# Optimization experiments

Hardware: AMD Instinct MI355X
Metric: run time of the kernel (lower is better)

The kernel has to match this reference:

```python
import jax, jax.numpy as jnp
import numpy as np

N_NODES = 32768
N_EDGES = 524288
EPS = 1e-5

def _layernorm(h):
    mu = jnp.mean(h, axis=-1, keepdims=True)
    var = jnp.var(h, axis=-1, keepdims=True)
    return (h - mu) / jnp.sqrt(var + EPS)

def _leaky_relu(h):
    return jnp.where(h >= 0, h, 0.01 * h)

def setup_inputs() -> dict:
    key = jax.random.key(0)
    ks = jax.random.split(key, 16)
    F, H, D = 256, 256, 1024
    x = jax.random.normal(ks[0], (N_NODES, F), dtype=jnp.float32)
    src = jax.random.randint(ks[1], (N_EDGES,), 0, N_NODES, dtype=jnp.int32)
    dst = jax.random.randint(ks[2], (N_EDGES,), 0, N_NODES, dtype=jnp.int32)
    dims = [F, H, H, H, D]
    params = {}
    for i in range(4):
        params[f"W{i+1}"] = jax.random.normal(ks[3 + i], (dims[i], dims[i + 1]), dtype=jnp.float32) * (1.0 / np.sqrt(dims[i]))
        params[f"b{i+1}"] = jnp.zeros((dims[i + 1],), dtype=jnp.float32)
    Wm = jax.random.normal(ks[8], (D, D), dtype=jnp.float32) * (1.0 / np.sqrt(D))
    bm = jnp.zeros((D,), dtype=jnp.float32)
    Ws = jax.random.normal(ks[9], (D, D), dtype=jnp.float32) * (1.0 / np.sqrt(D))
    bs = jnp.zeros((D,), dtype=jnp.float32)
    return dict(x=x, src=src, dst=dst, W1=params["W1"], b1=params["b1"], W2=params["W2"], b2=params["b2"], W3=params["W3"], b3=params["b3"], W4=params["W4"], b4=params["b4"], Wm=Wm, bm=bm, Ws=Ws, bs=bs, batch_b=128, nodes_per=256)

def reference(x, src, dst, W1, b1, W2, b2, W3, b3, W4, b4, Wm, bm, Ws, bs, batch_b, nodes_per):
    # DGL GraphConv norm='both': out = D_in^{-1/2} * A @ (D_out^{-1/2} * h) @ W + b
    ones = jnp.ones((src.shape[0],), dtype=x.dtype)
    out_deg = jax.ops.segment_sum(ones, src, num_segments=N_NODES)
    in_deg = jax.ops.segment_sum(ones, dst, num_segments=N_NODES)
    ns = jnp.where(out_deg > 0, jax.lax.rsqrt(out_deg), 1.0)[:, None]
    nd = jnp.where(in_deg > 0, jax.lax.rsqrt(in_deg), 1.0)[:, None]

    def gconv(h, W, b):
        if W.shape[0] <= W.shape[1]:  # aggregate first, then project (in <= out)
            m = (h * ns)[src]
            agg = jax.ops.segment_sum(m, dst, num_segments=N_NODES) * nd
            return agg @ W + b
        else:  # project first
            h = (h * ns) @ W
            agg = jax.ops.segment_sum(h[src], dst, num_segments=N_NODES) * nd
            return agg + b

    h = x
    for (W, b) in [(W1, b1), (W2, b2), (W3, b3), (W4, b4)]:
        h = _layernorm(_leaky_relu(gconv(h, W, b)))
    h = h.reshape(batch_b, nodes_per, -1)  # [B, N_per, D]
    h = jnp.mean(h, axis=1)                # AvePool over nodes
    h = _layernorm(h)
    mean = h @ Wm + bm
    log_std = h @ Ws + bs
    return (mean, log_std)
```

## Files before the change

kernel.cpp:

```cpp
#include <hip/hip_runtime.h>

#define N_NODES 32768
#define N_EDGES 524288

typedef __attribute__((ext_vector_type(8))) short short8;
typedef __attribute__((ext_vector_type(4))) float floatx4;

#define GLOBAL_AS __attribute__((address_space(1)))
#define LDS_AS __attribute__((address_space(3)))

__device__ __forceinline__ unsigned short f2bf(float x) {
    union { float f; unsigned u; } v; v.f = x;
    unsigned r = v.u + 0x7FFF + ((v.u >> 16) & 1);
    return (unsigned short)(r >> 16);
}
__device__ __forceinline__ float bf2f(unsigned short u) {
    union { unsigned u; float f; } v; v.u = ((unsigned)u) << 16;
    return v.f;
}


__global__ __launch_bounds__(256) void k_hist(const int* __restrict__ src,
                                              const int* __restrict__ dst,
                                              unsigned int* __restrict__ histOut32,
                                              unsigned int* __restrict__ histIn32) {
    __shared__ unsigned int hOut[8192];
    __shared__ unsigned int hIn[8192];
    int t = threadIdx.x, b = blockIdx.x;
    for (int i = t; i < 8192; i += 256) { hOut[i] = 0; hIn[i] = 0; }
    __syncthreads();
    int base = b * 4096;
    for (int i = t; i < 4096; i += 256) {
        int s = src[base + i], d = dst[base + i];
        atomicAdd(&hOut[s >> 2], 1u << ((s & 3) * 8));
        atomicAdd(&hIn[d >> 2], 1u << ((d & 3) * 8));
    }
    __syncthreads();
    for (int i = t; i < 8192; i += 256) {
        histOut32[b * 8192 + i] = hOut[i];
        histIn32[b * 8192 + i] = hIn[i];
    }
}

__global__ __launch_bounds__(256) void k_merge(const unsigned int* __restrict__ histOut32,
                                               const unsigned int* __restrict__ histIn32,
                                               unsigned int* __restrict__ pre32,
                                               int* __restrict__ in_deg,
                                               float* __restrict__ ns,
                                               float* __restrict__ nd) {
    int g = blockIdx.x * 256 + threadIdx.x;
    int ri0 = 0, ri1 = 0, ri2 = 0, ri3 = 0;
    for (int b = 0; b < 128; b++) {
        pre32[b * 8192 + g] = (unsigned)ri0 | ((unsigned)ri1 << 8) |
                              ((unsigned)ri2 << 16) | ((unsigned)ri3 << 24);
        unsigned int v = histIn32[b * 8192 + g];
        ri0 += v & 255; ri1 += (v >> 8) & 255; ri2 += (v >> 16) & 255; ri3 += (v >> 24) & 255;
    }
    in_deg[g * 4 + 0] = ri0; in_deg[g * 4 + 1] = ri1;
    in_deg[g * 4 + 2] = ri2; in_deg[g * 4 + 3] = ri3;
    nd[g * 4 + 0] = ri0 > 0 ? rsqrtf((float)ri0) : 1.0f;
    nd[g * 4 + 1] = ri1 > 0 ? rsqrtf((float)ri1) : 1.0f;
    nd[g * 4 + 2] = ri2 > 0 ? rsqrtf((float)ri2) : 1.0f;
    nd[g * 4 + 3] = ri3 > 0 ? rsqrtf((float)ri3) : 1.0f;
    int ro0 = 0, ro1 = 0, ro2 = 0, ro3 = 0;
    for (int b = 0; b < 128; b++) {
        unsigned int v = histOut32[b * 8192 + g];
        ro0 += v & 255; ro1 += (v >> 8) & 255; ro2 += (v >> 16) & 255; ro3 += (v >> 24) & 255;
    }
    ns[g * 4 + 0] = ro0 > 0 ? rsqrtf((float)ro0) : 1.0f;
    ns[g * 4 + 1] = ro1 > 0 ? rsqrtf((float)ro1) : 1.0f;
    ns[g * 4 + 2] = ro2 > 0 ? rsqrtf((float)ro2) : 1.0f;
    ns[g * 4 + 3] = ro3 > 0 ? rsqrtf((float)ro3) : 1.0f;
}

__global__ void k_scan(const int* __restrict__ in_deg, int* __restrict__ row_ptr) {
    __shared__ int part[1024];
    int t = threadIdx.x;
    int base = t * 32;
    int local[32];
    int s = 0;
    for (int i = 0; i < 32; i++) { local[i] = s; s += in_deg[base + i]; }
    part[t] = s;
    __syncthreads();
    for (int off = 1; off < 1024; off <<= 1) {
        int v = (t >= off) ? part[t - off] : 0;
        __syncthreads();
        part[t] += v;
        __syncthreads();
    }
    int prev = (t == 0) ? 0 : part[t - 1];
    for (int i = 0; i < 32; i++) row_ptr[base + i] = prev + local[i];
    if (t == 1023) row_ptr[N_NODES] = part[1023];
}

__global__ __launch_bounds__(256) void k_place(const int* __restrict__ src,
                                               const int* __restrict__ dst,
                                               const unsigned int* __restrict__ pre32,
                                               const int* __restrict__ row_ptr,
                                               int* __restrict__ csr_src) {
    __shared__ unsigned int cur[8192];
    int t = threadIdx.x, b = blockIdx.x;
    for (int i = t; i < 8192; i += 256) cur[i] = 0;
    __syncthreads();
    int base = b * 4096;
    const unsigned int* preb = pre32 + b * 8192;
    for (int i = t; i < 4096; i += 256) {
        int s = src[base + i], d = dst[base + i];
        int sh = (d & 3) * 8;
        unsigned int old = atomicAdd(&cur[d >> 2], 1u << sh);
        int rank = (old >> sh) & 255;
        int pb = (preb[d >> 2] >> sh) & 255;
        csr_src[row_ptr[d] + pb + rank] = s;
    }
}

struct TransDescs {
    const float* W[6];
    unsigned short* Wt[6];
    int K[6], N[6];
    int end[6];
};

__global__ __launch_bounds__(256) void k_transpose_all(TransDescs d) {
    int id = blockIdx.x, s = 0;
#pragma unroll
    for (int i = 0; i < 6; i++) if (id >= d.end[i]) s = i + 1;
    int base = (s == 0) ? 0 : d.end[s - 1];
    int t = id - base;
    int K = d.K[s], N = d.N[s];
    int ncols = N >> 5;
    int n0 = (t % ncols) * 32, k0 = (t / ncols) * 32;
    const float* W = d.W[s];
    unsigned short* Wt = d.Wt[s];
    __shared__ float tile[32][33];
    int tx = threadIdx.x & 31, ty = threadIdx.x >> 5;
    for (int r = 0; r < 32; r += 8)
        tile[ty + r][tx] = W[(size_t)(k0 + ty + r) * N + n0 + tx];
    __syncthreads();
    for (int r = 0; r < 32; r += 8)
        Wt[(size_t)(n0 + ty + r) * K + k0 + tx] = f2bf(tile[tx][ty + r]);
}

__global__ __launch_bounds__(256) void k_scale_x(const float* __restrict__ x,
                                                 const float* __restrict__ ns,
                                                 unsigned short* __restrict__ xsb) {
    int i = blockIdx.x * 256 + threadIdx.x;
    float4 v = ((const float4*)x)[i];
    int n = i >> 6;
    int f = (i & 63) * 4;
    float sc = ns[n];
    ushort4 o;
    o.x = f2bf(v.x * sc); o.y = f2bf(v.y * sc);
    o.z = f2bf(v.z * sc); o.w = f2bf(v.w * sc);
    size_t off = (size_t)(f >> 6) * (N_NODES * 64) + (size_t)n * 64 + (f & 63);
    *(ushort4*)(xsb + off) = o;
}

__global__ __launch_bounds__(128, 8) void k_aggregate(
        const unsigned short* __restrict__ hs,
        const int* __restrict__ row_ptr,
        const int* __restrict__ csr_src,
        const float* __restrict__ nd,
        unsigned short* __restrict__ aggb) {
    __shared__ int eIdx[512];
    __shared__ int rp[17];
    const int tid = threadIdx.x;
    const int n0 = blockIdx.x * 16;
    if (tid <= 16) rp[tid] = row_ptr[n0 + tid];
    __syncthreads();
    const int ebeg = rp[0];
    const int ecount = rp[16] - ebeg;
    const int ecached = ecount < 512 ? ecount : 512;
    for (int i = tid; i < ecached; i += 128) eIdx[i] = csr_src[ebeg + i];
    __syncthreads();

    const int nl = tid >> 3;
    const int fs = tid & 7;
    const int n = n0 + nl;
    const int beg = rp[nl] - ebeg, end = rp[nl + 1] - ebeg;
    const float sc = nd[n];

    auto sweep = [&](auto fetch) {
        for (int c = 0; c < 4; c++) {
            const unsigned short* hp = hs + (size_t)c * (N_NODES * 64) + fs * 8;
            float acc[8];
#pragma unroll
            for (int k = 0; k < 8; k++) acc[k] = 0.f;
            int e = beg;
            for (; e + 8 <= end; e += 8) {
                int s0 = fetch(e),     s1 = fetch(e + 1), s2 = fetch(e + 2), s3 = fetch(e + 3);
                int s4 = fetch(e + 4), s5 = fetch(e + 5), s6 = fetch(e + 6), s7 = fetch(e + 7);
                short8 v0 = *(const short8*)(hp + (size_t)s0 * 64);
                short8 v1 = *(const short8*)(hp + (size_t)s1 * 64);
                short8 v2 = *(const short8*)(hp + (size_t)s2 * 64);
                short8 v3 = *(const short8*)(hp + (size_t)s3 * 64);
                short8 v4 = *(const short8*)(hp + (size_t)s4 * 64);
                short8 v5 = *(const short8*)(hp + (size_t)s5 * 64);
                short8 v6 = *(const short8*)(hp + (size_t)s6 * 64);
                short8 v7 = *(const short8*)(hp + (size_t)s7 * 64);
#pragma unroll
                for (int k = 0; k < 8; k++)
                    acc[k] += ((bf2f((unsigned short)v0[k]) + bf2f((unsigned short)v1[k])) +
                               (bf2f((unsigned short)v2[k]) + bf2f((unsigned short)v3[k]))) +
                              ((bf2f((unsigned short)v4[k]) + bf2f((unsigned short)v5[k])) +
                               (bf2f((unsigned short)v6[k]) + bf2f((unsigned short)v7[k])));
            }
            for (; e + 2 <= end; e += 2) {
                int s0 = fetch(e), s1 = fetch(e + 1);
                short8 v0 = *(const short8*)(hp + (size_t)s0 * 64);
                short8 v1 = *(const short8*)(hp + (size_t)s1 * 64);
#pragma unroll
                for (int k = 0; k < 8; k++)
                    acc[k] += bf2f((unsigned short)v0[k]) + bf2f((unsigned short)v1[k]);
            }
            if (e < end) {
                int s = fetch(e);
                short8 v = *(const short8*)(hp + (size_t)s * 64);
#pragma unroll
                for (int k = 0; k < 8; k++) acc[k] += bf2f((unsigned short)v[k]);
            }
            short8 o;
#pragma unroll
            for (int k = 0; k < 8; k++) o[k] = (short)f2bf(acc[k] * sc);
            __builtin_nontemporal_store(o, (short8*)(aggb + (size_t)n * 256 + c * 64 + fs * 8));
        }
    };
    if (ecount <= 512)
        sweep([&](int e) { return eIdx[e]; });
    else
        sweep([&](int e) { return csr_src[ebeg + e]; });
}

__global__ __launch_bounds__(256, 2) void gemm_ln(
        const unsigned short* __restrict__ A, const unsigned short* __restrict__ Bt,
        const float* __restrict__ bias, const float* __restrict__ ns,
        unsigned short* __restrict__ hsb) {
    __shared__ __align__(16) unsigned short As[2][64 * 32];
    __shared__ __align__(16) unsigned short Bs[2][256 * 32];
    __shared__ float sSum[2][64], sSum2[2][64], sMa[64], sMb[64];
    const int tid = threadIdx.x;
    const int lane = tid & 63;
    const int w = tid >> 6;
    const int wr = (w >> 1) * 32;
    const int wc = (w & 1) * 128;
    const int rowBase = blockIdx.x * 64;
    const int K = 256;

    floatx4 acc[2][8];
#pragma unroll
    for (int i = 0; i < 2; i++)
#pragma unroll
        for (int j = 0; j < 8; j++) acc[i][j] = (floatx4){0.f, 0.f, 0.f, 0.f};

    const int pr = lane >> 3;
    const int uu = (lane & 7) ^ pr;
    const int rowInGrp = pr * 2 + (uu >> 2);
    const int kc = (uu & 3) * 8;
    const unsigned short* gA = A + (size_t)(rowBase + w * 16 + rowInGrp) * K + kc;
    const unsigned short* gB = Bt + (size_t)(w * 64 + rowInGrp) * K + kc;
    const int aBase = (w * 16) * 32;
    const int bBase = (w * 64) * 32;

    const int q = lane >> 4;
    const int ln = lane & 15;
    const int uf = (((ln & 1) << 2) | q) ^ ((ln >> 1) & 7);

#define STAGE(buf_, koff_)                                                               \
    {                                                                                    \
        unsigned short* lA = As[buf_] + aBase;                                           \
        unsigned short* lB = Bs[buf_] + bBase;                                           \
        __builtin_amdgcn_global_load_lds((const GLOBAL_AS short*)(gA + (koff_)),         \
                                         (LDS_AS short*)lA, 16, 0, 0);                   \
        __builtin_amdgcn_global_load_lds((const GLOBAL_AS short*)(gB + (koff_)),         \
                                         (LDS_AS short*)lB, 16, 0, 0);                   \
        __builtin_amdgcn_global_load_lds((const GLOBAL_AS short*)(gB + (koff_) + (size_t)16 * K), \
                                         (LDS_AS short*)(lB + 16 * 32), 16, 0, 0);       \
        __builtin_amdgcn_global_load_lds((const GLOBAL_AS short*)(gB + (koff_) + (size_t)32 * K), \
                                         (LDS_AS short*)(lB + 32 * 32), 16, 0, 0);       \
        __builtin_amdgcn_global_load_lds((const GLOBAL_AS short*)(gB + (koff_) + (size_t)48 * K), \
                                         (LDS_AS short*)(lB + 48 * 32), 16, 0, 0);       \
    }

    STAGE(0, 0)
    int buf = 0;
    for (int k0 = 0; k0 < K; k0 += 32) {
        __syncthreads();
        if (k0 + 32 < K) STAGE(buf ^ 1, k0 + 32)
        const unsigned short* rA = As[buf];
        const unsigned short* rB = Bs[buf];
        short8 af[2], bfr[8];
#pragma unroll
        for (int i = 0; i < 2; i++)
            af[i] = *(const short8*)(rA + (((wr + i * 16 + ln) >> 1) << 6) + uf * 8);
#pragma unroll
        for (int j = 0; j < 8; j++)
            bfr[j] = *(const short8*)(rB + (((wc + j * 16 + ln) >> 1) << 6) + uf * 8);
#pragma unroll
        for (int i = 0; i < 2; i++)
#pragma unroll
            for (int j = 0; j < 8; j++)
                acc[i][j] = __builtin_amdgcn_mfma_f32_16x16x32_bf16(af[i], bfr[j], acc[i][j], 0, 0, 0);
        buf ^= 1;
    }
#undef STAGE

    float bcol[8];
#pragma unroll
    for (int j = 0; j < 8; j++) bcol[j] = bias[wc + j * 16 + ln];
    const int wcIdx = w & 1;
#pragma unroll
    for (int i = 0; i < 2; i++) {
#pragma unroll
        for (int r = 0; r < 4; r++) {
            float s = 0.f, s2 = 0.f;
#pragma unroll
            for (int j = 0; j < 8; j++) {
                float v = acc[i][j][r] + bcol[j];
                v = v >= 0.f ? v : 0.01f * v;
                s += v; s2 += v * v;
            }
#pragma unroll
            for (int off = 8; off > 0; off >>= 1) {
                s += __shfl_down(s, off, 16);
                s2 += __shfl_down(s2, off, 16);
            }
            if (ln == 0) {
                int row = wr + i * 16 + q * 4 + r;
                sSum[wcIdx][row] = s;
                sSum2[wcIdx][row] = s2;
            }
        }
    }
    __syncthreads();
    if (tid < 64) {
        float mu = (sSum[0][tid] + sSum[1][tid]) * (1.0f / 256.0f);
        float var = (sSum2[0][tid] + sSum2[1][tid]) * (1.0f / 256.0f) - mu * mu;
        float rs = rsqrtf(var + 1e-5f);
        float nsv = ns[rowBase + tid];
        sMa[tid] = rs * nsv;
        sMb[tid] = -mu * rs * nsv;
    }
    __syncthreads();
#pragma unroll
    for (int i = 0; i < 2; i++) {
#pragma unroll
        for (int r = 0; r < 4; r++) {
            int row = wr + i * 16 + q * 4 + r;
            float a = sMa[row], bb = sMb[row];
#pragma unroll
            for (int j = 0; j < 8; j++) {
                float v = acc[i][j][r] + bcol[j];
                v = v >= 0.f ? v : 0.01f * v;
                int col = wc + j * 16 + ln;
                size_t off = (size_t)(col >> 6) * (N_NODES * 64) +
                             (size_t)(rowBase + row) * 64 + (col & 63);
                hsb[off] = f2bf(v * a + bb);
            }
        }
    }
}

template <bool LEAKY, bool OUT_BF16>
__global__ __launch_bounds__(256) void gemm_mfma(
        const unsigned short* __restrict__ A, const unsigned short* __restrict__ Bt,
        const float* __restrict__ bias,
        void* __restrict__ Cv,
        int M, int N, int K) {
    __shared__ __align__(16) unsigned short As[2][128 * 32];
    __shared__ __align__(16) unsigned short Bs[2][128 * 32];
    const int tid = threadIdx.x;
    const int lane = tid & 63;
    const int w = tid >> 6;
    const int wr = (w >> 1) * 64;
    const int wc = (w & 1) * 64;
    const int rowBase = blockIdx.x * 128;
    const int colBase = blockIdx.y * 128;

    floatx4 acc[4][4];
#pragma unroll
    for (int i = 0; i < 4; i++)
#pragma unroll
        for (int j = 0; j < 4; j++) acc[i][j] = (floatx4){0.f, 0.f, 0.f, 0.f};

    const int pr = lane >> 3;
    const int uu = (lane & 7) ^ pr;
    const int srow = w * 32 + pr * 2 + (uu >> 2);
    const int kc = (uu & 3) * 8;
    const unsigned short* gA = A + (size_t)(rowBase + srow) * K + kc;
    const unsigned short* gB = Bt + (size_t)(colBase + srow) * K + kc;
    const int wbase = (w * 32) * 32;

    const int q = lane >> 4;
    const int ln = lane & 15;
    const int uf = (((ln & 1) << 2) | q) ^ ((ln >> 1) & 7);

    {
        unsigned short* lA = As[0] + wbase;
        unsigned short* lB = Bs[0] + wbase;
        __builtin_amdgcn_global_load_lds((const GLOBAL_AS short*)(gA),
                                         (LDS_AS short*)lA, 16, 0, 0);
        __builtin_amdgcn_global_load_lds((const GLOBAL_AS short*)(gA + (size_t)16 * K),
                                         (LDS_AS short*)(lA + 16 * 32), 16, 0, 0);
        __builtin_amdgcn_global_load_lds((const GLOBAL_AS short*)(gB),
                                         (LDS_AS short*)lB, 16, 0, 0);
        __builtin_amdgcn_global_load_lds((const GLOBAL_AS short*)(gB + (size_t)16 * K),
                                         (LDS_AS short*)(lB + 16 * 32), 16, 0, 0);
    }

    int buf = 0;
    for (int k0 = 0; k0 < K; k0 += 32) {
        __syncthreads();
        if (k0 + 32 < K) {
            unsigned short* lA = As[buf ^ 1] + wbase;
            unsigned short* lB = Bs[buf ^ 1] + wbase;
            __builtin_amdgcn_global_load_lds((const GLOBAL_AS short*)(gA + k0 + 32),
                                             (LDS_AS short*)lA, 16, 0, 0);
            __builtin_amdgcn_global_load_lds((const GLOBAL_AS short*)(gA + k0 + 32 + (size_t)16 * K),
                                             (LDS_AS short*)(lA + 16 * 32), 16, 0, 0);
            __builtin_amdgcn_global_load_lds((const GLOBAL_AS short*)(gB + k0 + 32),
                                             (LDS_AS short*)lB, 16, 0, 0);
            __builtin_amdgcn_global_load_lds((const GLOBAL_AS short*)(gB + k0 + 32 + (size_t)16 * K),
                                             (LDS_AS short*)(lB + 16 * 32), 16, 0, 0);
        }
        const unsigned short* rA = As[buf];
        const unsigned short* rB = Bs[buf];
        short8 af[4], bfr[4];
#pragma unroll
        for (int i = 0; i < 4; i++)
            af[i] = *(const short8*)(rA + (((wr + i * 16 + ln) >> 1) << 6) + uf * 8);
#pragma unroll
        for (int j = 0; j < 4; j++)
            bfr[j] = *(const short8*)(rB + (((wc + j * 16 + ln) >> 1) << 6) + uf * 8);
#pragma unroll
        for (int i = 0; i < 4; i++)
#pragma unroll
            for (int j = 0; j < 4; j++)
                acc[i][j] = __builtin_amdgcn_mfma_f32_16x16x32_bf16(af[i], bfr[j], acc[i][j], 0, 0, 0);
        buf ^= 1;
    }
#pragma unroll
    for (int i = 0; i < 4; i++) {
#pragma unroll
        for (int j = 0; j < 4; j++) {
#pragma unroll
            for (int r = 0; r < 4; r++) {
                int row = rowBase + wr + i * 16 + q * 4 + r;
                int col = colBase + wc + j * 16 + ln;
                float v = acc[i][j][r] + bias[col];
                if (LEAKY) v = v >= 0.f ? v : 0.01f * v;
                if (OUT_BF16)
                    ((unsigned short*)Cv)[(size_t)row * N + col] = f2bf(v);
                else
                    ((float*)Cv)[(size_t)row * N + col] = v;
            }
        }
    }
}

__global__ __launch_bounds__(256) void gemm_heads(
        const unsigned short* __restrict__ A,
        const unsigned short* __restrict__ Bt,
        float* __restrict__ P) {
    __shared__ __align__(16) unsigned short As[2][128 * 32];
    __shared__ __align__(16) unsigned short Bs[2][128 * 32];
    const int tid = threadIdx.x;
    const int lane = tid & 63;
    const int w = tid >> 6;
    const int wr = (w >> 1) * 64;
    const int wc = (w & 1) * 64;
    const int colBase = blockIdx.x * 128;
    const int ks = blockIdx.y;
    const int K = 1024;

    floatx4 acc[4][4];
#pragma unroll
    for (int i = 0; i < 4; i++)
#pragma unroll
        for (int j = 0; j < 4; j++) acc[i][j] = (floatx4){0.f, 0.f, 0.f, 0.f};

    const int pr = lane >> 3;
    const int uu = (lane & 7) ^ pr;
    const int srow = w * 32 + pr * 2 + (uu >> 2);
    const int kc = (uu & 3) * 8;
    const unsigned short* gA = A + (size_t)srow * K + ks * 128 + kc;
    const unsigned short* gB = Bt + (size_t)(colBase + srow) * K + ks * 128 + kc;
    const int wbase = (w * 32) * 32;

    const int q = lane >> 4;
    const int ln = lane & 15;
    const int uf = (((ln & 1) << 2) | q) ^ ((ln >> 1) & 7);

    {
        unsigned short* lA = As[0] + wbase;
        unsigned short* lB = Bs[0] + wbase;
        __builtin_amdgcn_global_load_lds((const GLOBAL_AS short*)(gA),
                                         (LDS_AS short*)lA, 16, 0, 0);
        __builtin_amdgcn_global_load_lds((const GLOBAL_AS short*)(gA + (size_t)16 * K),
                                         (LDS_AS short*)(lA + 16 * 32), 16, 0, 0);
        __builtin_amdgcn_global_load_lds((const GLOBAL_AS short*)(gB),
                                         (LDS_AS short*)lB, 16, 0, 0);
        __builtin_amdgcn_global_load_lds((const GLOBAL_AS short*)(gB + (size_t)16 * K),
                                         (LDS_AS short*)(lB + 16 * 32), 16, 0, 0);
    }

    int buf = 0;
    for (int k0 = 0; k0 < 128; k0 += 32) {
        __syncthreads();
        if (k0 + 32 < 128) {
            unsigned short* lA = As[buf ^ 1] + wbase;
            unsigned short* lB = Bs[buf ^ 1] + wbase;
            __builtin_amdgcn_global_load_lds((const GLOBAL_AS short*)(gA + k0 + 32),
                                             (LDS_AS short*)lA, 16, 0, 0);
            __builtin_amdgcn_global_load_lds((const GLOBAL_AS short*)(gA + k0 + 32 + (size_t)16 * K),
                                             (LDS_AS short*)(lA + 16 * 32), 16, 0, 0);
            __builtin_amdgcn_global_load_lds((const GLOBAL_AS short*)(gB + k0 + 32),
                                             (LDS_AS short*)lB, 16, 0, 0);
            __builtin_amdgcn_global_load_lds((const GLOBAL_AS short*)(gB + k0 + 32 + (size_t)16 * K),
                                             (LDS_AS short*)(lB + 16 * 32), 16, 0, 0);
        }
        const unsigned short* rA = As[buf];
        const unsigned short* rB = Bs[buf];
        short8 af[4], bfr[4];
#pragma unroll
        for (int i = 0; i < 4; i++)
            af[i] = *(const short8*)(rA + (((wr + i * 16 + ln) >> 1) << 6) + uf * 8);
#pragma unroll
        for (int j = 0; j < 4; j++)
            bfr[j] = *(const short8*)(rB + (((wc + j * 16 + ln) >> 1) << 6) + uf * 8);
#pragma unroll
        for (int i = 0; i < 4; i++)
#pragma unroll
            for (int j = 0; j < 4; j++)
                acc[i][j] = __builtin_amdgcn_mfma_f32_16x16x32_bf16(af[i], bfr[j], acc[i][j], 0, 0, 0);
        buf ^= 1;
    }
    float* Pk = P + (size_t)ks * 128 * 2048;
#pragma unroll
    for (int i = 0; i < 4; i++) {
#pragma unroll
        for (int j = 0; j < 4; j++) {
#pragma unroll
            for (int r = 0; r < 4; r++) {
                int row = wr + i * 16 + q * 4 + r;
                int col = colBase + wc + j * 16 + ln;
                Pk[(size_t)row * 2048 + col] = acc[i][j][r];
            }
        }
    }
}

__global__ __launch_bounds__(256) void k_heads_reduce(
        const float* __restrict__ P, const float* __restrict__ bm,
        const float* __restrict__ bsd, float* __restrict__ out) {
    int idx = blockIdx.x * 256 + threadIdx.x;
    int row = idx >> 9;
    int col = (idx & 511) * 4;
    floatx4 s = (floatx4){0.f, 0.f, 0.f, 0.f};
#pragma unroll
    for (int p = 0; p < 8; p++)
        s += *(const floatx4*)(P + (size_t)p * 128 * 2048 + (size_t)row * 2048 + col);
    bool hi = col >= 1024;
    const float* bias = hi ? bsd : bm;
    int bc = hi ? col - 1024 : col;
    s += *(const floatx4*)(bias + bc);
    float* o = hi ? (out + (size_t)128 * 1024 + (size_t)row * 1024 + bc)
                  : (out + (size_t)row * 1024 + col);
    *(floatx4*)o = s;
}

__global__ __launch_bounds__(256) void k_lnpool(const unsigned short* __restrict__ h4,
                                                float* __restrict__ partial) {
    const int g = blockIdx.y, p = blockIdx.x;
    const int w = threadIdx.x >> 6, lane = threadIdx.x & 63;
    float acc[16];
#pragma unroll
    for (int k = 0; k < 16; k++) acc[k] = 0.f;
    for (int i = 0; i < 8; i++) {
        int node = (g * 8 + p) * 32 + w * 8 + i;
        const unsigned short* row = h4 + (size_t)node * 1024 + lane * 16;
        short8 a = *(const short8*)row;
        short8 b = *(const short8*)(row + 8);
        float v[16];
#pragma unroll
        for (int k = 0; k < 8; k++) v[k] = bf2f((unsigned short)a[k]);
#pragma unroll
        for (int k = 0; k < 8; k++) v[8 + k] = bf2f((unsigned short)b[k]);
        float s = 0.f, s2 = 0.f;
#pragma unroll
        for (int k = 0; k < 16; k++) { s += v[k]; s2 += v[k] * v[k]; }
#pragma unroll
        for (int off = 32; off > 0; off >>= 1) {
            s += __shfl_down(s, off);
            s2 += __shfl_down(s2, off);
        }
        s = __shfl(s, 0);
        s2 = __shfl(s2, 0);
        float mu = s * (1.0f / 1024.0f);
        float var = s2 * (1.0f / 1024.0f) - mu * mu;
        float rs = rsqrtf(var + 1e-5f);
#pragma unroll
        for (int k = 0; k < 16; k++) acc[k] += (v[k] - mu) * rs;
    }
    __shared__ float red[4][1024];
    float* my = red[w] + lane * 16;
#pragma unroll
    for (int k = 0; k < 16; k++) my[k] = acc[k];
    __syncthreads();
    int t = threadIdx.x;
    floatx4 o = (floatx4){0.f, 0.f, 0.f, 0.f};
#pragma unroll
    for (int w2 = 0; w2 < 4; w2++) {
        const floatx4 v = *(const floatx4*)(red[w2] + t * 4);
        o += v;
    }
    __builtin_nontemporal_store(o, (floatx4*)(partial + (size_t)(g * 8 + p) * 1024 + t * 4));
}

__global__ __launch_bounds__(256) void k_pool_final(const float* __restrict__ partial,
                                                    unsigned short* __restrict__ pooledb) {
    int g = blockIdx.x, t = threadIdx.x;
    int wave = t >> 6;
    float4 a = make_float4(0.f, 0.f, 0.f, 0.f);
    for (int p = 0; p < 8; p++) {
        float4 v = *(const float4*)(partial + (size_t)(g * 8 + p) * 1024 + t * 4);
        a.x += v.x; a.y += v.y; a.z += v.z; a.w += v.w;
    }
    const float invn = 1.0f / 256.0f;
    a.x *= invn; a.y *= invn; a.z *= invn; a.w *= invn;
    float s = a.x + a.y + a.z + a.w;
    float s2 = a.x * a.x + a.y * a.y + a.z * a.z + a.w * a.w;
#pragma unroll
    for (int off = 32; off > 0; off >>= 1) {
        s += __shfl_down(s, off);
        s2 += __shfl_down(s2, off);
    }
    __shared__ float ss[4], ss2[4];
    if ((t & 63) == 0) { ss[wave] = s; ss2[wave] = s2; }
    __syncthreads();
    if (t == 0) {
        float tt = 0.f, tt2 = 0.f;
        for (int w = 0; w < 4; w++) { tt += ss[w]; tt2 += ss2[w]; }
        float mu = tt / 1024.f;
        float var = tt2 / 1024.f - mu * mu;
        ss[0] = mu;
        ss2[0] = rsqrtf(var + 1e-5f);
    }
    __syncthreads();
    float mu = ss[0], inv = ss2[0];
    ushort4 o;
    o.x = f2bf((a.x - mu) * inv); o.y = f2bf((a.y - mu) * inv);
    o.z = f2bf((a.z - mu) * inv); o.w = f2bf((a.w - mu) * inv);
    *(ushort4*)(pooledb + (size_t)g * 1024 + t * 4) = o;
}

extern "C" void kernel_launch(void* const* d_in, const int* in_sizes, int n_in,
                              void* d_out, int out_size, void* d_ws, size_t ws_size,
                              hipStream_t stream) {
    const float* x  = (const float*)d_in[0];
    const int*   src = (const int*)d_in[1];
    const int*   dst = (const int*)d_in[2];
    const float* W1 = (const float*)d_in[3];  const float* b1 = (const float*)d_in[4];
    const float* W2 = (const float*)d_in[5];  const float* b2 = (const float*)d_in[6];
    const float* W3 = (const float*)d_in[7];  const float* b3 = (const float*)d_in[8];
    const float* W4 = (const float*)d_in[9];  const float* b4 = (const float*)d_in[10];
    const float* Wm = (const float*)d_in[11]; const float* bm = (const float*)d_in[12];
    const float* Wsd = (const float*)d_in[13]; const float* bsd = (const float*)d_in[14];
    float* out = (float*)d_out;

    char* w = (char*)d_ws;
    unsigned short* aggb = (unsigned short*)w; w += (size_t)N_NODES * 256 * 2;
    unsigned short* hsb  = (unsigned short*)w; w += (size_t)N_NODES * 256 * 2;
    unsigned short* h4b  = (unsigned short*)w; w += (size_t)N_NODES * 1024 * 2;
    float* partial = (float*)w; w += (size_t)128 * 8 * 1024 * 4;
    unsigned short* pooledb = (unsigned short*)w; w += (size_t)128 * 1024 * 2;
    unsigned short* W1t = (unsigned short*)w; w += (size_t)256 * 256 * 2;
    unsigned short* W2t = (unsigned short*)w; w += (size_t)256 * 256 * 2;
    unsigned short* W3t = (unsigned short*)w; w += (size_t)256 * 256 * 2;
    unsigned short* W4t = (unsigned short*)w; w += (size_t)256 * 1024 * 2;
    unsigned short* Wmt = (unsigned short*)w; w += (size_t)1024 * 1024 * 2;
    unsigned short* Wst = (unsigned short*)w; w += (size_t)1024 * 1024 * 2;
    float* ns     = (float*)w; w += (size_t)N_NODES * 4;
    float* nd     = (float*)w; w += (size_t)N_NODES * 4;
    unsigned int* histOut32 = (unsigned int*)w; w += (size_t)128 * 8192 * 4;
    unsigned int* histIn32  = (unsigned int*)w; w += (size_t)128 * 8192 * 4;
    unsigned int* pre32     = (unsigned int*)w; w += (size_t)128 * 8192 * 4;
    int* in_deg   = (int*)w;   w += (size_t)N_NODES * 4;
    int* row_ptr  = (int*)w;   w += (size_t)(N_NODES + 1) * 4;
    int* csr_src  = (int*)w;   w += (size_t)N_EDGES * 4;
    float* headp = (float*)histOut32;

    TransDescs td;
    td.W[0] = W1; td.W[1] = W2; td.W[2] = W3; td.W[3] = W4; td.W[4] = Wm; td.W[5] = Wsd;
    td.Wt[0] = W1t; td.Wt[1] = W2t; td.Wt[2] = W3t; td.Wt[3] = W4t; td.Wt[4] = Wmt; td.Wt[5] = Wst;
    td.K[0] = 256; td.K[1] = 256; td.K[2] = 256; td.K[3] = 256; td.K[4] = 1024; td.K[5] = 1024;
    td.N[0] = 256; td.N[1] = 256; td.N[2] = 256; td.N[3] = 1024; td.N[4] = 1024; td.N[5] = 1024;
    td.end[0] = 64; td.end[1] = 128; td.end[2] = 192; td.end[3] = 448; td.end[4] = 1472; td.end[5] = 2496;
    k_transpose_all<<<2496, 256, 0, stream>>>(td);

    k_hist<<<128, 256, 0, stream>>>(src, dst, histOut32, histIn32);
    k_merge<<<32, 256, 0, stream>>>(histOut32, histIn32, pre32, in_deg, ns, nd);
    k_scan<<<1, 1024, 0, stream>>>(in_deg, row_ptr);
    k_place<<<128, 256, 0, stream>>>(src, dst, pre32, row_ptr, csr_src);

    k_scale_x<<<N_NODES * 256 / 1024, 256, 0, stream>>>(x, ns, hsb);

    const unsigned short* Wts[3] = {W1t, W2t, W3t};
    const float* bs3[3] = {b1, b2, b3};
    for (int l = 0; l < 3; l++) {
        k_aggregate<<<N_NODES / 16, 128, 0, stream>>>(hsb, row_ptr, csr_src, nd, aggb);
        gemm_ln<<<N_NODES / 64, 256, 0, stream>>>(aggb, Wts[l], bs3[l], ns, hsb);
    }

    k_aggregate<<<N_NODES / 16, 128, 0, stream>>>(hsb, row_ptr, csr_src, nd, aggb);
    gemm_mfma<true, true><<<dim3(N_NODES / 128, 8), 256, 0, stream>>>(
        aggb, W4t, b4, h4b, N_NODES, 1024, 256);

    k_lnpool<<<dim3(8, 128), 256, 0, stream>>>(h4b, partial);
    k_pool_final<<<128, 256, 0, stream>>>(partial, pooledb);

    gemm_heads<<<dim3(16, 8), 256, 0, stream>>>(pooledb, Wmt, headp);
    k_heads_reduce<<<256, 256, 0, stream>>>(headp, bm, bsd, out);
}
```

Baseline: 395.0 us.

## Fuse neighbor aggregation with GEMM+LayerNorm for the first three GCN layers

Replaces the separate aggregate and gemm_ln kernels for layers 1-3 with one 512-thread kernel. Each block aggregates 64 destination rows into a swizzled LDS A tile, then runs the MFMA GEMM with bias, leaky-ReLU and LayerNorm directly on that tile. This removes the aggregated-activation round trip through global memory and one launch per layer. In exchange it needs ping-pong output buffers, since inputs are gathered from arbitrary nodes, and it uses much more LDS per block, which limits occupancy during the latency-bound gather.

```diff
diff --git a/kernel.cpp b/kernel.cpp
--- a/kernel.cpp
+++ b/kernel.cpp
@@ -156,29 +156,57 @@
     *(ushort4*)(xsb + off) = o;
 }
 
-__global__ __launch_bounds__(128, 8) void k_aggregate(
+__global__ __launch_bounds__(512, 4) void fused_layer(
         const unsigned short* __restrict__ hs,
         const int* __restrict__ row_ptr,
         const int* __restrict__ csr_src,
         const float* __restrict__ nd,
-        unsigned short* __restrict__ aggb) {
-    __shared__ int eIdx[512];
-    __shared__ int rp[17];
+        const unsigned short* __restrict__ Bt,
+        const float* __restrict__ bias,
+        const float* __restrict__ ns,
+        unsigned short* __restrict__ ho) {
+    __shared__ __align__(16) unsigned short At[8 * 2048];
+    __shared__ __align__(16) unsigned short Bs[2][256 * 32];
+    __shared__ int eIdx[2048];
+    __shared__ int rp[65];
+    __shared__ float sSum[4][64], sSum2[4][64], sMa[64], sMb[64];
     const int tid = threadIdx.x;
-    const int n0 = blockIdx.x * 16;
-    if (tid <= 16) rp[tid] = row_ptr[n0 + tid];
+    const int lane = tid & 63;
+    const int w = tid >> 6;
+    const int n0 = blockIdx.x * 64;
+    const int K = 256;
+
+    const int pr = lane >> 3;
+    const int uu = (lane & 7) ^ pr;
+    const int rowInGrp = pr * 2 + (uu >> 2);
+    const int kc = (uu & 3) * 8;
+    const unsigned short* gB = Bt + (size_t)(w * 32 + rowInGrp) * K + kc;
+    const int bBase = (w * 32) * 32;
+#define STAGEB(buf_, koff_)                                                              \
+    {                                                                                    \
+        unsigned short* lB = Bs[buf_] + bBase;                                           \
+        __builtin_amdgcn_global_load_lds((const GLOBAL_AS short*)(gB + (koff_)),         \
+                                         (LDS_AS short*)lB, 16, 0, 0);                   \
+        __builtin_amdgcn_global_load_lds((const GLOBAL_AS short*)(gB + (koff_) + (size_t)16 * K), \
+                                         (LDS_AS short*)(lB + 16 * 32), 16, 0, 0);       \
+    }
+    STAGEB(0, 0)
+
+    if (tid <= 64) rp[tid] = row_ptr[n0 + tid];
     __syncthreads();
     const int ebeg = rp[0];
-    const int ecount = rp[16] - ebeg;
-    const int ecached = ecount < 512 ? ecount : 512;
-    for (int i = tid; i < ecached; i += 128) eIdx[i] = csr_src[ebeg + i];
-    __syncthreads();
-
-    const int nl = tid >> 3;
+    const int ecount = rp[64] - ebeg;
+    const int ecached = ecount < 2048 ? ecount : 2048;
+    for (int i = tid; i < ecached; i += 512) eIdx[i] = csr_src[ebeg + i];
+    __syncthreads();
+
+    const int r = tid >> 3;
     const int fs = tid & 7;
-    const int n = n0 + nl;
-    const int beg = rp[nl] - ebeg, end = rp[nl + 1] - ebeg;
-    const float sc = nd[n];
+    const int beg = rp[r] - ebeg, end = rp[r + 1] - ebeg;
+    const float sc = nd[n0 + r];
+    const int rowpair = r >> 1;
+    unsigned short* atp = At + rowpair * 64 +
+                          (((((r & 1) << 2) | (fs & 3)) ^ (rowpair & 7)) << 3);
 
     auto sweep = [&](auto fetch) {
         for (int c = 0; c < 4; c++) {
@@ -222,6 +250,171 @@
             short8 o;
 #pragma unroll
             for (int k = 0; k < 8; k++) o[k] = (short)f2bf(acc[k] * sc);
+            *(short8*)(atp + (c * 2 + (fs >> 2)) * 2048) = o;
+        }
+    };
+    if (ecount <= 2048)
+        sweep([&](int e) { return eIdx[e]; });
+    else
+        sweep([&](int e) { return csr_src[ebeg + e]; });
+
+    const int wr = (w >> 2) * 32;
+    const int wc = (w & 3) * 64;
+    floatx4 acc2[2][4];
+#pragma unroll
+    for (int i = 0; i < 2; i++)
+#pragma unroll
+        for (int j = 0; j < 4; j++) acc2[i][j] = (floatx4){0.f, 0.f, 0.f, 0.f};
+    const int q = lane >> 4;
+    const int ln = lane & 15;
+    const int uf = (((ln & 1) << 2) | q) ^ ((ln >> 1) & 7);
+
+    int buf = 0;
+    for (int k0 = 0; k0 < K; k0 += 32) {
+        __syncthreads();
+        if (k0 + 32 < K) STAGEB(buf ^ 1, k0 + 32)
+        const unsigned short* rA = At + (k0 >> 5) * 2048;
+        const unsigned short* rB = Bs[buf];
+        short8 af[2], bfr[4];
+#pragma unroll
+        for (int i = 0; i < 2; i++)
+            af[i] = *(const short8*)(rA + (((wr + i * 16 + ln) >> 1) << 6) + uf * 8);
+#pragma unroll
+        for (int j = 0; j < 4; j++)
+            bfr[j] = *(const short8*)(rB + (((wc + j * 16 + ln) >> 1) << 6) + uf * 8);
+#pragma unroll
+        for (int i = 0; i < 2; i++)
+#pragma unroll
+            for (int j = 0; j < 4; j++)
+                acc2[i][j] = __builtin_amdgcn_mfma_f32_16x16x32_bf16(af[i], bfr[j], acc2[i][j], 0, 0, 0);
+        buf ^= 1;
+    }
+#undef STAGEB
+
+    float bcol[4];
+#pragma unroll
+    for (int j = 0; j < 4; j++) bcol[j] = bias[wc + j * 16 + ln];
+    const int wcIdx = w & 3;
+#pragma unroll
+    for (int i = 0; i < 2; i++) {
+#pragma unroll
+        for (int rr = 0; rr < 4; rr++) {
+            float s = 0.f, s2 = 0.f;
+#pragma unroll
+            for (int j = 0; j < 4; j++) {
+                float v = acc2[i][j][rr] + bcol[j];
+                v = v >= 0.f ? v : 0.01f * v;
+                s += v; s2 += v * v;
+            }
+#pragma unroll
+            for (int off = 8; off > 0; off >>= 1) {
+                s += __shfl_down(s, off, 16);
+                s2 += __shfl_down(s2, off, 16);
+            }
+            if (ln == 0) {
+                int row = wr + i * 16 + q * 4 + rr;
+                sSum[wcIdx][row] = s;
+                sSum2[wcIdx][row] = s2;
+            }
+        }
+    }
+    __syncthreads();
+    if (tid < 64) {
+        float su = sSum[0][tid] + sSum[1][tid] + sSum[2][tid] + sSum[3][tid];
+        float su2 = sSum2[0][tid] + sSum2[1][tid] + sSum2[2][tid] + sSum2[3][tid];
+        float mu = su * (1.0f / 256.0f);
+        float var = su2 * (1.0f / 256.0f) - mu * mu;
+        float rs = rsqrtf(var + 1e-5f);
+        float nsv = ns[n0 + tid];
+        sMa[tid] = rs * nsv;
+        sMb[tid] = -mu * rs * nsv;
+    }
+    __syncthreads();
+#pragma unroll
+    for (int i = 0; i < 2; i++) {
+#pragma unroll
+        for (int rr = 0; rr < 4; rr++) {
+            int row = wr + i * 16 + q * 4 + rr;
+            float a = sMa[row], bb = sMb[row];
+#pragma unroll
+            for (int j = 0; j < 4; j++) {
+                float v = acc2[i][j][rr] + bcol[j];
+                v = v >= 0.f ? v : 0.01f * v;
+                int col = wc + j * 16 + ln;
+                size_t off = (size_t)(col >> 6) * (N_NODES * 64) +
+                             (size_t)(n0 + row) * 64 + (col & 63);
+                ho[off] = f2bf(v * a + bb);
+            }
+        }
+    }
+}
+
+__global__ __launch_bounds__(128, 8) void k_aggregate(
+        const unsigned short* __restrict__ hs,
+        const int* __restrict__ row_ptr,
+        const int* __restrict__ csr_src,
+        const float* __restrict__ nd,
+        unsigned short* __restrict__ aggb) {
+    __shared__ int eIdx[512];
+    __shared__ int rp[17];
+    const int tid = threadIdx.x;
+    const int n0 = blockIdx.x * 16;
+    if (tid <= 16) rp[tid] = row_ptr[n0 + tid];
+    __syncthreads();
+    const int ebeg = rp[0];
+    const int ecount = rp[16] - ebeg;
+    const int ecached = ecount < 512 ? ecount : 512;
+    for (int i = tid; i < ecached; i += 128) eIdx[i] = csr_src[ebeg + i];
+    __syncthreads();
+
+    const int nl = tid >> 3;
+    const int fs = tid & 7;
+    const int n = n0 + nl;
+    const int beg = rp[nl] - ebeg, end = rp[nl + 1] - ebeg;
+    const float sc = nd[n];
+
+    auto sweep = [&](auto fetch) {
+        for (int c = 0; c < 4; c++) {
+            const unsigned short* hp = hs + (size_t)c * (N_NODES * 64) + fs * 8;
+            float acc[8];
+#pragma unroll
+            for (int k = 0; k < 8; k++) acc[k] = 0.f;
+            int e = beg;
+            for (; e + 8 <= end; e += 8) {
+                int s0 = fetch(e),     s1 = fetch(e + 1), s2 = fetch(e + 2), s3 = fetch(e + 3);
+                int s4 = fetch(e + 4), s5 = fetch(e + 5), s6 = fetch(e + 6), s7 = fetch(e + 7);
+                short8 v0 = *(const short8*)(hp + (size_t)s0 * 64);
+                short8 v1 = *(const short8*)(hp + (size_t)s1 * 64);
+                short8 v2 = *(const short8*)(hp + (size_t)s2 * 64);
+                short8 v3 = *(const short8*)(hp + (size_t)s3 * 64);
+                short8 v4 = *(const short8*)(hp + (size_t)s4 * 64);
+                short8 v5 = *(const short8*)(hp + (size_t)s5 * 64);
+                short8 v6 = *(const short8*)(hp + (size_t)s6 * 64);
+                short8 v7 = *(const short8*)(hp + (size_t)s7 * 64);
+#pragma unroll
+                for (int k = 0; k < 8; k++)
+                    acc[k] += ((bf2f((unsigned short)v0[k]) + bf2f((unsigned short)v1[k])) +
+                               (bf2f((unsigned short)v2[k]) + bf2f((unsigned short)v3[k]))) +
+                              ((bf2f((unsigned short)v4[k]) + bf2f((unsigned short)v5[k])) +
+                               (bf2f((unsigned short)v6[k]) + bf2f((unsigned short)v7[k])));
+            }
+            for (; e + 2 <= end; e += 2) {
+                int s0 = fetch(e), s1 = fetch(e + 1);
+                short8 v0 = *(const short8*)(hp + (size_t)s0 * 64);
+                short8 v1 = *(const short8*)(hp + (size_t)s1 * 64);
+#pragma unroll
+                for (int k = 0; k < 8; k++)
+                    acc[k] += bf2f((unsigned short)v0[k]) + bf2f((unsigned short)v1[k]);
+            }
+            if (e < end) {
+                int s = fetch(e);
+                short8 v = *(const short8*)(hp + (size_t)s * 64);
+#pragma unroll
+                for (int k = 0; k < 8; k++) acc[k] += bf2f((unsigned short)v[k]);
+            }
+            short8 o;
+#pragma unroll
+            for (int k = 0; k < 8; k++) o[k] = (short)f2bf(acc[k] * sc);
             __builtin_nontemporal_store(o, (short8*)(aggb + (size_t)n * 256 + c * 64 + fs * 8));
         }
     };
@@ -229,135 +422,6 @@
         sweep([&](int e) { return eIdx[e]; });
     else
         sweep([&](int e) { return csr_src[ebeg + e]; });
-}
-
-__global__ __launch_bounds__(256, 2) void gemm_ln(
-        const unsigned short* __restrict__ A, const unsigned short* __restrict__ Bt,
-        const float* __restrict__ bias, const float* __restrict__ ns,
-        unsigned short* __restrict__ hsb) {
-    __shared__ __align__(16) unsigned short As[2][64 * 32];
-    __shared__ __align__(16) unsigned short Bs[2][256 * 32];
-    __shared__ float sSum[2][64], sSum2[2][64], sMa[64], sMb[64];
-    const int tid = threadIdx.x;
-    const int lane = tid & 63;
-    const int w = tid >> 6;
-    const int wr = (w >> 1) * 32;
-    const int wc = (w & 1) * 128;
-    const int rowBase = blockIdx.x * 64;
-    const int K = 256;
-
-    floatx4 acc[2][8];
-#pragma unroll
-    for (int i = 0; i < 2; i++)
-#pragma unroll
-        for (int j = 0; j < 8; j++) acc[i][j] = (floatx4){0.f, 0.f, 0.f, 0.f};
-
-    const int pr = lane >> 3;
-    const int uu = (lane & 7) ^ pr;
-    const int rowInGrp = pr * 2 + (uu >> 2);
-    const int kc = (uu & 3) * 8;
-    const unsigned short* gA = A + (size_t)(rowBase + w * 16 + rowInGrp) * K + kc;
-    const unsigned short* gB = Bt + (size_t)(w * 64 + rowInGrp) * K + kc;
-    const int aBase = (w * 16) * 32;
-    const int bBase = (w * 64) * 32;
-
-    const int q = lane >> 4;
-    const int ln = lane & 15;
-    const int uf = (((ln & 1) << 2) | q) ^ ((ln >> 1) & 7);
-
-#define STAGE(buf_, koff_)                                                               \
-    {                                                                                    \
-        unsigned short* lA = As[buf_] + aBase;                                           \
-        unsigned short* lB = Bs[buf_] + bBase;                                           \
-        __builtin_amdgcn_global_load_lds((const GLOBAL_AS short*)(gA + (koff_)),         \
-                                         (LDS_AS short*)lA, 16, 0, 0);                   \
-        __builtin_amdgcn_global_load_lds((const GLOBAL_AS short*)(gB + (koff_)),         \
-                                         (LDS_AS short*)lB, 16, 0, 0);                   \
-        __builtin_amdgcn_global_load_lds((const GLOBAL_AS short*)(gB + (koff_) + (size_t)16 * K), \
-                                         (LDS_AS short*)(lB + 16 * 32), 16, 0, 0);       \
-        __builtin_amdgcn_global_load_lds((const GLOBAL_AS short*)(gB + (koff_) + (size_t)32 * K), \
-                                         (LDS_AS short*)(lB + 32 * 32), 16, 0, 0);       \
-        __builtin_amdgcn_global_load_lds((const GLOBAL_AS short*)(gB + (koff_) + (size_t)48 * K), \
-                                         (LDS_AS short*)(lB + 48 * 32), 16, 0, 0);       \
-    }
-
-    STAGE(0, 0)
-    int buf = 0;
-    for (int k0 = 0; k0 < K; k0 += 32) {
-        __syncthreads();
-        if (k0 + 32 < K) STAGE(buf ^ 1, k0 + 32)
-        const unsigned short* rA = As[buf];
-        const unsigned short* rB = Bs[buf];
-        short8 af[2], bfr[8];
-#pragma unroll
-        for (int i = 0; i < 2; i++)
-            af[i] = *(const short8*)(rA + (((wr + i * 16 + ln) >> 1) << 6) + uf * 8);
-#pragma unroll
-        for (int j = 0; j < 8; j++)
-            bfr[j] = *(const short8*)(rB + (((wc + j * 16 + ln) >> 1) << 6) + uf * 8);
-#pragma unroll
-        for (int i = 0; i < 2; i++)
-#pragma unroll
-            for (int j = 0; j < 8; j++)
-                acc[i][j] = __builtin_amdgcn_mfma_f32_16x16x32_bf16(af[i], bfr[j], acc[i][j], 0, 0, 0);
-        buf ^= 1;
-    }
-#undef STAGE
-
-    float bcol[8];
-#pragma unroll
-    for (int j = 0; j < 8; j++) bcol[j] = bias[wc + j * 16 + ln];
-    const int wcIdx = w & 1;
-#pragma unroll
-    for (int i = 0; i < 2; i++) {
-#pragma unroll
-        for (int r = 0; r < 4; r++) {
-            float s = 0.f, s2 = 0.f;
-#pragma unroll
-            for (int j = 0; j < 8; j++) {
-                float v = acc[i][j][r] + bcol[j];
-                v = v >= 0.f ? v : 0.01f * v;
-                s += v; s2 += v * v;
-            }
-#pragma unroll
-            for (int off = 8; off > 0; off >>= 1) {
-                s += __shfl_down(s, off, 16);
-                s2 += __shfl_down(s2, off, 16);
-            }
-            if (ln == 0) {
-                int row = wr + i * 16 + q * 4 + r;
-                sSum[wcIdx][row] = s;
-                sSum2[wcIdx][row] = s2;
-            }
-        }
-    }
-    __syncthreads();
-    if (tid < 64) {
-        float mu = (sSum[0][tid] + sSum[1][tid]) * (1.0f / 256.0f);
-        float var = (sSum2[0][tid] + sSum2[1][tid]) * (1.0f / 256.0f) - mu * mu;
-        float rs = rsqrtf(var + 1e-5f);
-        float nsv = ns[rowBase + tid];
-        sMa[tid] = rs * nsv;
-        sMb[tid] = -mu * rs * nsv;
-    }
-    __syncthreads();
-#pragma unroll
-    for (int i = 0; i < 2; i++) {
-#pragma unroll
-        for (int r = 0; r < 4; r++) {
-            int row = wr + i * 16 + q * 4 + r;
-            float a = sMa[row], bb = sMb[row];
-#pragma unroll
-            for (int j = 0; j < 8; j++) {
-                float v = acc[i][j][r] + bcol[j];
-                v = v >= 0.f ? v : 0.01f * v;
-                int col = wc + j * 16 + ln;
-                size_t off = (size_t)(col >> 6) * (N_NODES * 64) +
-                             (size_t)(rowBase + row) * 64 + (col & 63);
-                hsb[off] = f2bf(v * a + bb);
-            }
-        }
-    }
 }
 
 template <bool LEAKY, bool OUT_BF16>
@@ -669,7 +733,8 @@
 
     char* w = (char*)d_ws;
     unsigned short* aggb = (unsigned short*)w; w += (size_t)N_NODES * 256 * 2;
-    unsigned short* hsb  = (unsigned short*)w; w += (size_t)N_NODES * 256 * 2;
+    unsigned short* hsbA = (unsigned short*)w; w += (size_t)N_NODES * 256 * 2;
+    unsigned short* hsbB = (unsigned short*)w; w += (size_t)N_NODES * 256 * 2;
     unsigned short* h4b  = (unsigned short*)w; w += (size_t)N_NODES * 1024 * 2;
     float* partial = (float*)w; w += (size_t)128 * 8 * 1024 * 4;
     unsigned short* pooledb = (unsigned short*)w; w += (size_t)128 * 1024 * 2;
@@ -702,16 +767,19 @@
     k_scan<<<1, 1024, 0, stream>>>(in_deg, row_ptr);
     k_place<<<128, 256, 0, stream>>>(src, dst, pre32, row_ptr, csr_src);
 
-    k_scale_x<<<N_NODES * 256 / 1024, 256, 0, stream>>>(x, ns, hsb);
+    k_scale_x<<<N_NODES * 256 / 1024, 256, 0, stream>>>(x, ns, hsbA);
 
     const unsigned short* Wts[3] = {W1t, W2t, W3t};
     const float* bs3[3] = {b1, b2, b3};
+    unsigned short* tin = hsbA;
+    unsigned short* tout = hsbB;
     for (int l = 0; l < 3; l++) {
-        k_aggregate<<<N_NODES / 16, 128, 0, stream>>>(hsb, row_ptr, csr_src, nd, aggb);
-        gemm_ln<<<N_NODES / 64, 256, 0, stream>>>(aggb, Wts[l], bs3[l], ns, hsb);
-    }
-
-    k_aggregate<<<N_NODES / 16, 128, 0, stream>>>(hsb, row_ptr, csr_src, nd, aggb);
+        fused_layer<<<N_NODES / 64, 512, 0, stream>>>(tin, row_ptr, csr_src, nd,
+                                                      Wts[l], bs3[l], ns, tout);
+        unsigned short* tmp = tin; tin = tout; tout = tmp;
+    }
+
+    k_aggregate<<<N_NODES / 16, 128, 0, stream>>>(tin, row_ptr, csr_src, nd, aggb);
     gemm_mfma<true, true><<<dim3(N_NODES / 128, 8), 256, 0, stream>>>(
         aggb, W4t, b4, h4b, N_NODES, 1024, 256);
 
```

Result: faster. 363.5 us (-8.0%).
